# Optimization experiments

Measured on AMD Instinct MI355X. Metric: run time of the kernel, lower is better.

The kernel has to match this reference:

```python
import jax, jax.numpy as jnp
import numpy as np

N_NODES = 100000
N_EDGES = 1600000
D_IN = 64
D_OUT = 64


def setup_inputs() -> dict:
    key = jax.random.key(0)
    k1, k2, k3, k4 = jax.random.split(key, 4)
    x = jax.random.normal(k1, (N_NODES, D_IN), dtype=jnp.float32)
    edge_index = jax.random.randint(k2, (2, N_EDGES), 0, N_NODES, dtype=jnp.int64)
    W = jax.random.normal(k3, (D_OUT, D_IN), dtype=jnp.float32) * (1.0 / np.sqrt(D_IN))
    b = jax.random.normal(k4, (D_OUT,), dtype=jnp.float32) * 0.01
    return {"x": x, "edge_index": edge_index, "W": W, "b": b}


def reference(x, edge_index, W, b):
    num_nodes = x.shape[0]
    row, col = edge_index[0], edge_index[1]
    # degree of each node as a destination (scatter_add of ones over row)
    deg = jax.ops.segment_sum(jnp.ones(row.shape[0], dtype=x.dtype), row,
                              num_segments=num_nodes)
    # deg^-0.5 with inf (deg==0) replaced by 0
    deg_inv_sqrt = jnp.where(deg > 0, jax.lax.rsqrt(jnp.maximum(deg, 1.0)) * jnp.where(deg > 0, 1.0, 0.0), 0.0)
    deg_inv_sqrt = jnp.where(deg > 0, deg ** -0.5, 0.0)
    # gather source features, scale by source norm, scatter-add to destinations
    weighted = x[col] * deg_inv_sqrt[col][:, None]          # [E, D_IN]
    agg = jax.ops.segment_sum(weighted, row, num_segments=num_nodes)  # [N, D_IN]
    agg = agg * deg_inv_sqrt[:, None]
    # linear + relu (torch Linear: y = agg @ W.T + b)
    return jax.nn.relu(agg @ W.T + b)
```

## Files before the change

kernel.cpp:

```cpp
#include <hip/hip_runtime.h>

#define N_NODES 100000
#define N_EDGES 1600000
#define D 64

#define CSHIFT 7
#define CNODES 128
#define NCB 782
#define CAPC 2560
#define COLBITS 17
#define COLMASK 0x1FFFF

#define CHUNKA 2048
#define EPTA 8
#define NCHA 782
#define XBLKS 1563

#define CCUR_OFF   0
#define CPAIRS_OFF 3200
#define RS_OFF     8010880
#define DG_OFF     8410880
#define DINV_OFF   8810880
#define Y_OFF      9210880

typedef float fvec4 __attribute__((ext_vector_type(4)));
typedef __attribute__((ext_vector_type(8))) short bf16x8;
typedef __attribute__((ext_vector_type(4))) float f32x4;

__device__ __forceinline__ float bf2f(unsigned short u) {
    return __uint_as_float(((unsigned)u) << 16);
}
__device__ __forceinline__ unsigned f2bf(float f) {
    unsigned bits = __float_as_uint(f);
    return (bits + 0x7FFFu + ((bits >> 16) & 1u)) >> 16;
}

__global__ __launch_bounds__(256) void fat_kernel(
        const float* __restrict__ x, const float* __restrict__ W,
        const int* __restrict__ row, const int* __restrict__ col,
        int* __restrict__ ccur, int* __restrict__ cpairs,
        unsigned short* __restrict__ y) {
    __shared__ int lcnt[NCB];
    int t = threadIdx.x;
    if (blockIdx.x < XBLKS) {
        int wave = t >> 6, lane = t & 63;
        int n0w = blockIdx.x * 64 + wave * 16;
        if (n0w >= N_NODES) return;
        int lm = lane & 15;
        int g  = lane >> 4;
        bf16x8 ahi[2], alo[2];
        const float* xr = x + (size_t)(n0w + lm) * D + g * 8;
#pragma unroll
        for (int ks = 0; ks < 2; ++ks) {
            float4 fa = *(const float4*)(xr + ks * 32);
            float4 fb = *(const float4*)(xr + ks * 32 + 4);
            float f[8] = {fa.x, fa.y, fa.z, fa.w, fb.x, fb.y, fb.z, fb.w};
#pragma unroll
            for (int j = 0; j < 8; ++j) {
                unsigned hb = f2bf(f[j]);
                float r = f[j] - bf2f((unsigned short)hb);
                ahi[ks][j] = (short)hb;
                alo[ks][j] = (short)f2bf(r);
            }
        }
#pragma unroll
        for (int jt = 0; jt < 4; ++jt) {
            const float* wr = W + (size_t)(jt * 16 + lm) * D + g * 8;
            bf16x8 whi[2], wlo[2];
#pragma unroll
            for (int ks = 0; ks < 2; ++ks) {
                float4 fa = *(const float4*)(wr + ks * 32);
                float4 fb = *(const float4*)(wr + ks * 32 + 4);
                float f[8] = {fa.x, fa.y, fa.z, fa.w, fb.x, fb.y, fb.z, fb.w};
#pragma unroll
                for (int j = 0; j < 8; ++j) {
                    unsigned hb = f2bf(f[j]);
                    float r = f[j] - bf2f((unsigned short)hb);
                    whi[ks][j] = (short)hb;
                    wlo[ks][j] = (short)f2bf(r);
                }
            }
            f32x4 acc = {0.0f, 0.0f, 0.0f, 0.0f};
#pragma unroll
            for (int ks = 0; ks < 2; ++ks) {
                acc = __builtin_amdgcn_mfma_f32_16x16x32_bf16(ahi[ks], whi[ks], acc, 0, 0, 0);
                acc = __builtin_amdgcn_mfma_f32_16x16x32_bf16(alo[ks], whi[ks], acc, 0, 0, 0);
                acc = __builtin_amdgcn_mfma_f32_16x16x32_bf16(ahi[ks], wlo[ks], acc, 0, 0, 0);
            }
#pragma unroll
            for (int r = 0; r < 4; ++r) {
                int n = n0w + g * 4 + r;
                y[(size_t)n * D + jt * 16 + lm] = (unsigned short)f2bf(acc[r]);
            }
        }
    } else {
        int base = (blockIdx.x - XBLKS) * CHUNKA;
        for (int i = t; i < NCB; i += 256) lcnt[i] = 0;
        __syncthreads();
        int r[EPTA], c[EPTA], pos[EPTA];
#pragma unroll
        for (int i = 0; i < EPTA; ++i) {
            int e = base + i * 256 + t;
            if (e < N_EDGES) {
                r[i] = row[e];
                c[i] = col[e];
                pos[i] = atomicAdd(&lcnt[r[i] >> CSHIFT], 1);
            } else r[i] = -1;
        }
        __syncthreads();
        for (int i = t; i < NCB; i += 256) {
            int cc = lcnt[i];
            lcnt[i] = cc ? atomicAdd(&ccur[i], cc) : 0;
        }
        __syncthreads();
#pragma unroll
        for (int i = 0; i < EPTA; ++i) {
            if (r[i] >= 0) {
                int cb = r[i] >> CSHIFT;
                int p = lcnt[cb] + pos[i];
                if (p < CAPC)
                    cpairs[cb * CAPC + p] = ((r[i] & (CNODES - 1)) << COLBITS) | c[i];
            }
        }
    }
}

__global__ __launch_bounds__(512) void scatB_kernel(const int* __restrict__ ccur,
                                                    int* __restrict__ cpairs,
                                                    int* __restrict__ rs,
                                                    int* __restrict__ dg,
                                                    float* __restrict__ dinv) {
    __shared__ int epk[CAPC];
    __shared__ int hist[CNODES];
    __shared__ int sc[CNODES];
    __shared__ int cur[CNODES];
    int t = threadIdx.x;
    int cb = blockIdx.x;
    int cnt = ccur[cb]; if (cnt > CAPC) cnt = CAPC;
    int base = cb * CAPC;
    if (t < CNODES) hist[t] = 0;
    __syncthreads();
    for (int i = t; i < cnt; i += 512) {
        int p = cpairs[base + i];
        epk[i] = p;
        atomicAdd(&hist[p >> COLBITS], 1);
    }
    __syncthreads();
    if (t < CNODES) sc[t] = hist[t];
    __syncthreads();
    for (int off = 1; off < CNODES; off <<= 1) {
        int v = (t < CNODES && t >= off) ? sc[t - off] : 0;
        __syncthreads();
        if (t < CNODES) sc[t] += v;
        __syncthreads();
    }
    if (t < CNODES) {
        int ex = sc[t] - hist[t];
        cur[t] = ex;
        int n = (cb << CSHIFT) + t;
        if (n < N_NODES) {
            rs[n] = base + ex;
            dg[n] = hist[t];
            dinv[n] = (hist[t] > 0) ? rsqrtf((float)hist[t]) : 0.0f;
        }
    }
    __syncthreads();
    for (int i = t; i < cnt; i += 512) {
        int p = epk[i];
        int pos = atomicAdd(&cur[p >> COLBITS], 1);
        cpairs[base + pos] = p & COLMASK;
    }
}

__global__ __launch_bounds__(256) void mega_kernel(
        const int* __restrict__ cols, const int* __restrict__ rs,
        const int* __restrict__ dg, const float* __restrict__ dinv,
        const unsigned short* __restrict__ y,
        const float* __restrict__ bias, float* __restrict__ out) {
    int t = threadIdx.x;
    int wave = t >> 6, lane = t & 63;
    int g = lane >> 3, q = lane & 7;
    int n = blockIdx.x * 32 + wave * 8 + g;
    int s = rs[n], d = dg[n];
    float bj[8];
    {
        float4 b0 = *(const float4*)(bias + q * 8);
        float4 b1 = *(const float4*)(bias + q * 8 + 4);
        bj[0] = b0.x; bj[1] = b0.y; bj[2] = b0.z; bj[3] = b0.w;
        bj[4] = b1.x; bj[5] = b1.y; bj[6] = b1.z; bj[7] = b1.w;
    }
    float a[8];
#pragma unroll
    for (int j = 0; j < 8; ++j) a[j] = 0.0f;
    int c4[4];
#pragma unroll
    for (int u = 0; u < 4; ++u) c4[u] = (u < d) ? cols[s + u] : 0;
    for (int k = 0; k < d; k += 4) {
        uint4 v[4];
        float dvl[4];
#pragma unroll
        for (int u = 0; u < 4; ++u) {
            if (k + u < d) {
                int c = c4[u];
                dvl[u] = dinv[c];
                v[u] = *(const uint4*)(y + (size_t)c * D + q * 8);
            }
        }
#pragma unroll
        for (int u = 0; u < 4; ++u) {
            int e2 = k + 4 + u;
            c4[u] = (e2 < d) ? cols[s + e2] : 0;
        }
#pragma unroll
        for (int u = 0; u < 4; ++u) {
            if (k + u < d) {
                float dvu = dvl[u];
                a[0] = fmaf(dvu, __uint_as_float(v[u].x << 16),        a[0]);
                a[1] = fmaf(dvu, __uint_as_float(v[u].x & 0xffff0000u), a[1]);
                a[2] = fmaf(dvu, __uint_as_float(v[u].y << 16),        a[2]);
                a[3] = fmaf(dvu, __uint_as_float(v[u].y & 0xffff0000u), a[3]);
                a[4] = fmaf(dvu, __uint_as_float(v[u].z << 16),        a[4]);
                a[5] = fmaf(dvu, __uint_as_float(v[u].z & 0xffff0000u), a[5]);
                a[6] = fmaf(dvu, __uint_as_float(v[u].w << 16),        a[6]);
                a[7] = fmaf(dvu, __uint_as_float(v[u].w & 0xffff0000u), a[7]);
            }
        }
    }
    float dvn = dinv[n];
    fvec4 r0, r1;
    r0.x = fmaxf(fmaf(dvn, a[0], bj[0]), 0.0f);
    r0.y = fmaxf(fmaf(dvn, a[1], bj[1]), 0.0f);
    r0.z = fmaxf(fmaf(dvn, a[2], bj[2]), 0.0f);
    r0.w = fmaxf(fmaf(dvn, a[3], bj[3]), 0.0f);
    r1.x = fmaxf(fmaf(dvn, a[4], bj[4]), 0.0f);
    r1.y = fmaxf(fmaf(dvn, a[5], bj[5]), 0.0f);
    r1.z = fmaxf(fmaf(dvn, a[6], bj[6]), 0.0f);
    r1.w = fmaxf(fmaf(dvn, a[7], bj[7]), 0.0f);
    __builtin_nontemporal_store(r0, (fvec4*)(out + (size_t)n * D + q * 8));
    __builtin_nontemporal_store(r1, (fvec4*)(out + (size_t)n * D + q * 8 + 4));
}

extern "C" void kernel_launch(void* const* d_in, const int* in_sizes, int n_in,
                              void* d_out, int out_size, void* d_ws, size_t ws_size,
                              hipStream_t stream) {
    const float* x    = (const float*)d_in[0];
    const int*   eidx = (const int*)d_in[1];
    const float* W    = (const float*)d_in[2];
    const float* b    = (const float*)d_in[3];
    float* out = (float*)d_out;
    char* ws = (char*)d_ws;

    const int* row = eidx;
    const int* col = eidx + N_EDGES;

    int* ccur   = (int*)(ws + CCUR_OFF);
    int* cpairs = (int*)(ws + CPAIRS_OFF);
    int* rs     = (int*)(ws + RS_OFF);
    int* dg     = (int*)(ws + DG_OFF);
    float* dinv = (float*)(ws + DINV_OFF);
    unsigned short* y = (unsigned short*)(ws + Y_OFF);

    hipMemsetAsync(ccur, 0, NCB * sizeof(int), stream);
    fat_kernel<<<XBLKS + NCHA, 256, 0, stream>>>(x, W, row, col, ccur, cpairs, y);
    scatB_kernel<<<NCB, 512, 0, stream>>>(ccur, cpairs, rs, dg, dinv);
    mega_kernel<<<3125, 256, 0, stream>>>(cpairs, rs, dg, dinv, y, b, out);
}
```

Before: 169.9 us.

## Replace bucketed CSR build with global-atomic degree count, scan, and scatter

Replaces the two-level bucketed CSR construction (per-chunk LDS histograms into fixed-capacity coarse buckets, then a per-bucket local sort) with a global degree histogram made of global atomics, a three-kernel prefix scan, and a scatter pass that places each edge with a per-node global atomic. This removes the capacity limit and the intermediate packing, at the cost of three extra kernel launches and many contended global atomics on random node indices. The aggregation kernel's gather unroll also grows from 4 to 8 neighbours per step to keep more loads in flight, which raises register pressure.

Result: slower. 286.2 us (+68.5%).

```diff
diff --git a/kernel.cpp b/kernel.cpp
--- a/kernel.cpp
+++ b/kernel.cpp
@@ -2,26 +2,21 @@
 
 #define N_NODES 100000
 #define N_EDGES 1600000
+#define NE4 400000
 #define D 64
 
-#define CSHIFT 7
-#define CNODES 128
-#define NCB 782
-#define CAPC 2560
-#define COLBITS 17
-#define COLMASK 0x1FFFF
-
-#define CHUNKA 2048
-#define EPTA 8
-#define NCHA 782
 #define XBLKS 1563
-
-#define CCUR_OFF   0
-#define CPAIRS_OFF 3200
-#define RS_OFF     8010880
-#define DG_OFF     8410880
-#define DINV_OFF   8810880
-#define Y_OFF      9210880
+#define HBLKS 391
+#define NSB 391
+
+#define DG_OFF    0
+#define CUR_OFF   401408
+#define RS_OFF    802816
+#define DINV_OFF  1204224
+#define BSUM_OFF  1605632
+#define BOFF_OFF  1607232
+#define CP_OFF    1608832
+#define Y_OFF     8008832
 
 typedef float fvec4 __attribute__((ext_vector_type(4)));
 typedef __attribute__((ext_vector_type(8))) short bf16x8;
@@ -37,138 +32,150 @@
 
 __global__ __launch_bounds__(256) void fat_kernel(
         const float* __restrict__ x, const float* __restrict__ W,
-        const int* __restrict__ row, const int* __restrict__ col,
-        int* __restrict__ ccur, int* __restrict__ cpairs,
+        const int* __restrict__ row, int* __restrict__ dg,
         unsigned short* __restrict__ y) {
-    __shared__ int lcnt[NCB];
-    int t = threadIdx.x;
-    if (blockIdx.x < XBLKS) {
-        int wave = t >> 6, lane = t & 63;
-        int n0w = blockIdx.x * 64 + wave * 16;
-        if (n0w >= N_NODES) return;
-        int lm = lane & 15;
-        int g  = lane >> 4;
-        bf16x8 ahi[2], alo[2];
-        const float* xr = x + (size_t)(n0w + lm) * D + g * 8;
+    int t = threadIdx.x;
+    if (blockIdx.x < HBLKS) {
+        const int4* r4 = (const int4*)row;
+        int base4 = blockIdx.x * 1024;
+#pragma unroll
+        for (int i = 0; i < 4; ++i) {
+            int i4 = base4 + i * 256 + t;
+            if (i4 < NE4) {
+                int4 rv = r4[i4];
+                atomicAdd(&dg[rv.x], 1);
+                atomicAdd(&dg[rv.y], 1);
+                atomicAdd(&dg[rv.z], 1);
+                atomicAdd(&dg[rv.w], 1);
+            }
+        }
+        return;
+    }
+    int wave = t >> 6, lane = t & 63;
+    int n0w = (blockIdx.x - HBLKS) * 64 + wave * 16;
+    if (n0w >= N_NODES) return;
+    int lm = lane & 15;
+    int g  = lane >> 4;
+    bf16x8 ahi[2], alo[2];
+    const float* xr = x + (size_t)(n0w + lm) * D + g * 8;
+#pragma unroll
+    for (int ks = 0; ks < 2; ++ks) {
+        float4 fa = *(const float4*)(xr + ks * 32);
+        float4 fb = *(const float4*)(xr + ks * 32 + 4);
+        float f[8] = {fa.x, fa.y, fa.z, fa.w, fb.x, fb.y, fb.z, fb.w};
+#pragma unroll
+        for (int j = 0; j < 8; ++j) {
+            unsigned hb = f2bf(f[j]);
+            float r = f[j] - bf2f((unsigned short)hb);
+            ahi[ks][j] = (short)hb;
+            alo[ks][j] = (short)f2bf(r);
+        }
+    }
+#pragma unroll
+    for (int jt = 0; jt < 4; ++jt) {
+        const float* wr = W + (size_t)(jt * 16 + lm) * D + g * 8;
+        bf16x8 whi[2], wlo[2];
 #pragma unroll
         for (int ks = 0; ks < 2; ++ks) {
-            float4 fa = *(const float4*)(xr + ks * 32);
-            float4 fb = *(const float4*)(xr + ks * 32 + 4);
+            float4 fa = *(const float4*)(wr + ks * 32);
+            float4 fb = *(const float4*)(wr + ks * 32 + 4);
             float f[8] = {fa.x, fa.y, fa.z, fa.w, fb.x, fb.y, fb.z, fb.w};
 #pragma unroll
             for (int j = 0; j < 8; ++j) {
                 unsigned hb = f2bf(f[j]);
                 float r = f[j] - bf2f((unsigned short)hb);
-                ahi[ks][j] = (short)hb;
-                alo[ks][j] = (short)f2bf(r);
-            }
-        }
-#pragma unroll
-        for (int jt = 0; jt < 4; ++jt) {
-            const float* wr = W + (size_t)(jt * 16 + lm) * D + g * 8;
-            bf16x8 whi[2], wlo[2];
-#pragma unroll
-            for (int ks = 0; ks < 2; ++ks) {
-                float4 fa = *(const float4*)(wr + ks * 32);
-                float4 fb = *(const float4*)(wr + ks * 32 + 4);
-                float f[8] = {fa.x, fa.y, fa.z, fa.w, fb.x, fb.y, fb.z, fb.w};
-#pragma unroll
-                for (int j = 0; j < 8; ++j) {
-                    unsigned hb = f2bf(f[j]);
-                    float r = f[j] - bf2f((unsigned short)hb);
-                    whi[ks][j] = (short)hb;
-                    wlo[ks][j] = (short)f2bf(r);
-                }
-            }
-            f32x4 acc = {0.0f, 0.0f, 0.0f, 0.0f};
-#pragma unroll
-            for (int ks = 0; ks < 2; ++ks) {
-                acc = __builtin_amdgcn_mfma_f32_16x16x32_bf16(ahi[ks], whi[ks], acc, 0, 0, 0);
-                acc = __builtin_amdgcn_mfma_f32_16x16x32_bf16(alo[ks], whi[ks], acc, 0, 0, 0);
-                acc = __builtin_amdgcn_mfma_f32_16x16x32_bf16(ahi[ks], wlo[ks], acc, 0, 0, 0);
-            }
-#pragma unroll
-            for (int r = 0; r < 4; ++r) {
-                int n = n0w + g * 4 + r;
-                y[(size_t)n * D + jt * 16 + lm] = (unsigned short)f2bf(acc[r]);
-            }
-        }
-    } else {
-        int base = (blockIdx.x - XBLKS) * CHUNKA;
-        for (int i = t; i < NCB; i += 256) lcnt[i] = 0;
-        __syncthreads();
-        int r[EPTA], c[EPTA], pos[EPTA];
-#pragma unroll
-        for (int i = 0; i < EPTA; ++i) {
-            int e = base + i * 256 + t;
-            if (e < N_EDGES) {
-                r[i] = row[e];
-                c[i] = col[e];
-                pos[i] = atomicAdd(&lcnt[r[i] >> CSHIFT], 1);
-            } else r[i] = -1;
-        }
-        __syncthreads();
-        for (int i = t; i < NCB; i += 256) {
-            int cc = lcnt[i];
-            lcnt[i] = cc ? atomicAdd(&ccur[i], cc) : 0;
-        }
-        __syncthreads();
-#pragma unroll
-        for (int i = 0; i < EPTA; ++i) {
-            if (r[i] >= 0) {
-                int cb = r[i] >> CSHIFT;
-                int p = lcnt[cb] + pos[i];
-                if (p < CAPC)
-                    cpairs[cb * CAPC + p] = ((r[i] & (CNODES - 1)) << COLBITS) | c[i];
-            }
-        }
-    }
-}
-
-__global__ __launch_bounds__(512) void scatB_kernel(const int* __restrict__ ccur,
-                                                    int* __restrict__ cpairs,
+                whi[ks][j] = (short)hb;
+                wlo[ks][j] = (short)f2bf(r);
+            }
+        }
+        f32x4 acc = {0.0f, 0.0f, 0.0f, 0.0f};
+#pragma unroll
+        for (int ks = 0; ks < 2; ++ks) {
+            acc = __builtin_amdgcn_mfma_f32_16x16x32_bf16(ahi[ks], whi[ks], acc, 0, 0, 0);
+            acc = __builtin_amdgcn_mfma_f32_16x16x32_bf16(alo[ks], whi[ks], acc, 0, 0, 0);
+            acc = __builtin_amdgcn_mfma_f32_16x16x32_bf16(ahi[ks], wlo[ks], acc, 0, 0, 0);
+        }
+#pragma unroll
+        for (int r = 0; r < 4; ++r) {
+            int n = n0w + g * 4 + r;
+            y[(size_t)n * D + jt * 16 + lm] = (unsigned short)f2bf(acc[r]);
+        }
+    }
+}
+
+__global__ __launch_bounds__(256) void scan1_kernel(const int* __restrict__ dg,
+                                                    int* __restrict__ bsum) {
+    __shared__ int red[4];
+    int t = threadIdx.x;
+    int n = blockIdx.x * 256 + t;
+    int v = (n < N_NODES) ? dg[n] : 0;
+#pragma unroll
+    for (int m = 1; m < 64; m <<= 1) v += __shfl_xor(v, m);
+    if ((t & 63) == 0) red[t >> 6] = v;
+    __syncthreads();
+    if (t == 0) bsum[blockIdx.x] = red[0] + red[1] + red[2] + red[3];
+}
+
+__global__ __launch_bounds__(512) void scan2_kernel(const int* __restrict__ bsum,
+                                                    int* __restrict__ boff) {
+    __shared__ int ar[512];
+    int t = threadIdx.x;
+    int v = (t < NSB) ? bsum[t] : 0;
+    ar[t] = v;
+    __syncthreads();
+    for (int off = 1; off < 512; off <<= 1) {
+        int u = (t >= off) ? ar[t - off] : 0;
+        __syncthreads();
+        ar[t] += u;
+        __syncthreads();
+    }
+    if (t < NSB) boff[t] = ar[t] - v;
+}
+
+__global__ __launch_bounds__(256) void scan3_kernel(const int* __restrict__ dg,
+                                                    const int* __restrict__ boff,
                                                     int* __restrict__ rs,
-                                                    int* __restrict__ dg,
+                                                    int* __restrict__ cur,
                                                     float* __restrict__ dinv) {
-    __shared__ int epk[CAPC];
-    __shared__ int hist[CNODES];
-    __shared__ int sc[CNODES];
-    __shared__ int cur[CNODES];
-    int t = threadIdx.x;
-    int cb = blockIdx.x;
-    int cnt = ccur[cb]; if (cnt > CAPC) cnt = CAPC;
-    int base = cb * CAPC;
-    if (t < CNODES) hist[t] = 0;
+    __shared__ int ar[256];
+    int t = threadIdx.x;
+    int n = blockIdx.x * 256 + t;
+    int d = (n < N_NODES) ? dg[n] : 0;
+    ar[t] = d;
     __syncthreads();
-    for (int i = t; i < cnt; i += 512) {
-        int p = cpairs[base + i];
-        epk[i] = p;
-        atomicAdd(&hist[p >> COLBITS], 1);
-    }
-    __syncthreads();
-    if (t < CNODES) sc[t] = hist[t];
-    __syncthreads();
-    for (int off = 1; off < CNODES; off <<= 1) {
-        int v = (t < CNODES && t >= off) ? sc[t - off] : 0;
-        __syncthreads();
-        if (t < CNODES) sc[t] += v;
-        __syncthreads();
-    }
-    if (t < CNODES) {
-        int ex = sc[t] - hist[t];
-        cur[t] = ex;
-        int n = (cb << CSHIFT) + t;
-        if (n < N_NODES) {
-            rs[n] = base + ex;
-            dg[n] = hist[t];
-            dinv[n] = (hist[t] > 0) ? rsqrtf((float)hist[t]) : 0.0f;
-        }
-    }
-    __syncthreads();
-    for (int i = t; i < cnt; i += 512) {
-        int p = epk[i];
-        int pos = atomicAdd(&cur[p >> COLBITS], 1);
-        cpairs[base + pos] = p & COLMASK;
+    for (int off = 1; off < 256; off <<= 1) {
+        int u = (t >= off) ? ar[t - off] : 0;
+        __syncthreads();
+        ar[t] += u;
+        __syncthreads();
+    }
+    if (n < N_NODES) {
+        int r = boff[blockIdx.x] + ar[t] - d;
+        rs[n] = r;
+        cur[n] = r;
+        dinv[n] = (d > 0) ? rsqrtf((float)d) : 0.0f;
+    }
+}
+
+__global__ __launch_bounds__(256) void scat_kernel(const int* __restrict__ row,
+                                                   const int* __restrict__ col,
+                                                   int* __restrict__ cur,
+                                                   int* __restrict__ cpairs) {
+    int t = threadIdx.x;
+    const int4* r4 = (const int4*)row;
+    const int4* c4 = (const int4*)col;
+    int base4 = blockIdx.x * 1024;
+#pragma unroll
+    for (int i = 0; i < 4; ++i) {
+        int i4 = base4 + i * 256 + t;
+        if (i4 < NE4) {
+            int4 rv = r4[i4];
+            int4 cv = c4[i4];
+            int p0 = atomicAdd(&cur[rv.x], 1); cpairs[p0] = cv.x;
+            int p1 = atomicAdd(&cur[rv.y], 1); cpairs[p1] = cv.y;
+            int p2 = atomicAdd(&cur[rv.z], 1); cpairs[p2] = cv.z;
+            int p3 = atomicAdd(&cur[rv.w], 1); cpairs[p3] = cv.w;
+        }
     }
 }
 
@@ -192,36 +199,36 @@
     float a[8];
 #pragma unroll
     for (int j = 0; j < 8; ++j) a[j] = 0.0f;
-    int c4[4];
-#pragma unroll
-    for (int u = 0; u < 4; ++u) c4[u] = (u < d) ? cols[s + u] : 0;
-    for (int k = 0; k < d; k += 4) {
-        uint4 v[4];
-        float dvl[4];
-#pragma unroll
-        for (int u = 0; u < 4; ++u) {
+    int c8[8];
+#pragma unroll
+    for (int u = 0; u < 8; ++u) c8[u] = (u < d) ? cols[s + u] : 0;
+    for (int k = 0; k < d; k += 8) {
+        uint4 v[8];
+        float dv8[8];
+#pragma unroll
+        for (int u = 0; u < 8; ++u) {
             if (k + u < d) {
-                int c = c4[u];
-                dvl[u] = dinv[c];
+                int c = c8[u];
+                dv8[u] = dinv[c];
                 v[u] = *(const uint4*)(y + (size_t)c * D + q * 8);
             }
         }
 #pragma unroll
-        for (int u = 0; u < 4; ++u) {
-            int e2 = k + 4 + u;
-            c4[u] = (e2 < d) ? cols[s + e2] : 0;
-        }
-#pragma unroll
-        for (int u = 0; u < 4; ++u) {
+        for (int u = 0; u < 8; ++u) {
+            int e2 = k + 8 + u;
+            c8[u] = (e2 < d) ? cols[s + e2] : 0;
+        }
+#pragma unroll
+        for (int u = 0; u < 8; ++u) {
             if (k + u < d) {
-                float dvu = dvl[u];
-                a[0] = fmaf(dvu, __uint_as_float(v[u].x << 16),        a[0]);
+                float dvu = dv8[u];
+                a[0] = fmaf(dvu, __uint_as_float(v[u].x << 16),         a[0]);
                 a[1] = fmaf(dvu, __uint_as_float(v[u].x & 0xffff0000u), a[1]);
-                a[2] = fmaf(dvu, __uint_as_float(v[u].y << 16),        a[2]);
+                a[2] = fmaf(dvu, __uint_as_float(v[u].y << 16),         a[2]);
                 a[3] = fmaf(dvu, __uint_as_float(v[u].y & 0xffff0000u), a[3]);
-                a[4] = fmaf(dvu, __uint_as_float(v[u].z << 16),        a[4]);
+                a[4] = fmaf(dvu, __uint_as_float(v[u].z << 16),         a[4]);
                 a[5] = fmaf(dvu, __uint_as_float(v[u].z & 0xffff0000u), a[5]);
-                a[6] = fmaf(dvu, __uint_as_float(v[u].w << 16),        a[6]);
+                a[6] = fmaf(dvu, __uint_as_float(v[u].w << 16),         a[6]);
                 a[7] = fmaf(dvu, __uint_as_float(v[u].w & 0xffff0000u), a[7]);
             }
         }
@@ -253,15 +260,20 @@
     const int* row = eidx;
     const int* col = eidx + N_EDGES;
 
-    int* ccur   = (int*)(ws + CCUR_OFF);
-    int* cpairs = (int*)(ws + CPAIRS_OFF);
+    int* dg     = (int*)(ws + DG_OFF);
+    int* cur    = (int*)(ws + CUR_OFF);
     int* rs     = (int*)(ws + RS_OFF);
-    int* dg     = (int*)(ws + DG_OFF);
     float* dinv = (float*)(ws + DINV_OFF);
+    int* bsum   = (int*)(ws + BSUM_OFF);
+    int* boff   = (int*)(ws + BOFF_OFF);
+    int* cpairs = (int*)(ws + CP_OFF);
     unsigned short* y = (unsigned short*)(ws + Y_OFF);
 
-    hipMemsetAsync(ccur, 0, NCB * sizeof(int), stream);
-    fat_kernel<<<XBLKS + NCHA, 256, 0, stream>>>(x, W, row, col, ccur, cpairs, y);
-    scatB_kernel<<<NCB, 512, 0, stream>>>(ccur, cpairs, rs, dg, dinv);
+    hipMemsetAsync(dg, 0, N_NODES * sizeof(int), stream);
+    fat_kernel<<<HBLKS + XBLKS, 256, 0, stream>>>(x, W, row, dg, y);
+    scan1_kernel<<<NSB, 256, 0, stream>>>(dg, bsum);
+    scan2_kernel<<<1, 512, 0, stream>>>(bsum, boff);
+    scan3_kernel<<<NSB, 256, 0, stream>>>(dg, boff, rs, cur, dinv);
+    scat_kernel<<<HBLKS, 256, 0, stream>>>(row, col, cur, cpairs);
     mega_kernel<<<3125, 256, 0, stream>>>(cpairs, rs, dg, dinv, y, b, out);
 }
```

## Restructure edge bucketing into larger int4-vectorized blocks and unroll gather by eight

Applied to the files above, without the earlier changes.

The edge-bucketing part of the fused kernel now processes 8192 edges per block with int4 loads, and is placed before the matmul blocks so it is scheduled first. Each block counts per-bucket totals in a first pass, reserves global offsets once, then rereads the edges and scatters them, so per-block global atomics drop and more edges share each reservation. The gather loop in the aggregation kernel is unrolled from 4 to 8 neighbors to keep more loads in flight. The cost is reading row twice and fewer, longer scatter blocks, plus higher register pressure in the gather.

Measured after the change: 152.1 us. 10.5% less time.

```diff
diff --git a/kernel.cpp b/kernel.cpp
--- a/kernel.cpp
+++ b/kernel.cpp
@@ -2,6 +2,7 @@
 
 #define N_NODES 100000
 #define N_EDGES 1600000
+#define NE4 400000
 #define D 64
 
 #define CSHIFT 7
@@ -11,9 +12,8 @@
 #define COLBITS 17
 #define COLMASK 0x1FFFF
 
-#define CHUNKA 2048
-#define EPTA 8
-#define NCHA 782
+#define EPB 8192
+#define SBLKS 196
 #define XBLKS 1563
 
 #define CCUR_OFF   0
@@ -41,86 +41,100 @@
         int* __restrict__ ccur, int* __restrict__ cpairs,
         unsigned short* __restrict__ y) {
     __shared__ int lcnt[NCB];
+    __shared__ int lbase[NCB];
     int t = threadIdx.x;
-    if (blockIdx.x < XBLKS) {
-        int wave = t >> 6, lane = t & 63;
-        int n0w = blockIdx.x * 64 + wave * 16;
-        if (n0w >= N_NODES) return;
-        int lm = lane & 15;
-        int g  = lane >> 4;
-        bf16x8 ahi[2], alo[2];
-        const float* xr = x + (size_t)(n0w + lm) * D + g * 8;
+    if (blockIdx.x < SBLKS) {
+        const int4* r4 = (const int4*)row;
+        const int4* c4 = (const int4*)col;
+        int base4 = blockIdx.x * (EPB / 4);
+        for (int i = t; i < NCB; i += 256) lcnt[i] = 0;
+        __syncthreads();
+#pragma unroll
+        for (int i = 0; i < EPB / 1024; ++i) {
+            int i4 = base4 + i * 256 + t;
+            if (i4 < NE4) {
+                int4 rv = r4[i4];
+                atomicAdd(&lcnt[rv.x >> CSHIFT], 1);
+                atomicAdd(&lcnt[rv.y >> CSHIFT], 1);
+                atomicAdd(&lcnt[rv.z >> CSHIFT], 1);
+                atomicAdd(&lcnt[rv.w >> CSHIFT], 1);
+            }
+        }
+        __syncthreads();
+        for (int i = t; i < NCB; i += 256) {
+            int cc = lcnt[i];
+            lbase[i] = cc ? atomicAdd(&ccur[i], cc) : 0;
+            lcnt[i] = 0;
+        }
+        __syncthreads();
+#pragma unroll
+        for (int i = 0; i < EPB / 1024; ++i) {
+            int i4 = base4 + i * 256 + t;
+            if (i4 < NE4) {
+                int4 rv = r4[i4];
+                int4 cv = c4[i4];
+                int b0 = rv.x >> CSHIFT, b1 = rv.y >> CSHIFT;
+                int b2 = rv.z >> CSHIFT, b3 = rv.w >> CSHIFT;
+                int p0 = lbase[b0] + atomicAdd(&lcnt[b0], 1);
+                int p1 = lbase[b1] + atomicAdd(&lcnt[b1], 1);
+                int p2 = lbase[b2] + atomicAdd(&lcnt[b2], 1);
+                int p3 = lbase[b3] + atomicAdd(&lcnt[b3], 1);
+                if (p0 < CAPC) cpairs[(size_t)b0 * CAPC + p0] = ((rv.x & (CNODES - 1)) << COLBITS) | cv.x;
+                if (p1 < CAPC) cpairs[(size_t)b1 * CAPC + p1] = ((rv.y & (CNODES - 1)) << COLBITS) | cv.y;
+                if (p2 < CAPC) cpairs[(size_t)b2 * CAPC + p2] = ((rv.z & (CNODES - 1)) << COLBITS) | cv.z;
+                if (p3 < CAPC) cpairs[(size_t)b3 * CAPC + p3] = ((rv.w & (CNODES - 1)) << COLBITS) | cv.w;
+            }
+        }
+        return;
+    }
+    int wave = t >> 6, lane = t & 63;
+    int n0w = (blockIdx.x - SBLKS) * 64 + wave * 16;
+    if (n0w >= N_NODES) return;
+    int lm = lane & 15;
+    int g  = lane >> 4;
+    bf16x8 ahi[2], alo[2];
+    const float* xr = x + (size_t)(n0w + lm) * D + g * 8;
+#pragma unroll
+    for (int ks = 0; ks < 2; ++ks) {
+        float4 fa = *(const float4*)(xr + ks * 32);
+        float4 fb = *(const float4*)(xr + ks * 32 + 4);
+        float f[8] = {fa.x, fa.y, fa.z, fa.w, fb.x, fb.y, fb.z, fb.w};
+#pragma unroll
+        for (int j = 0; j < 8; ++j) {
+            unsigned hb = f2bf(f[j]);
+            float r = f[j] - bf2f((unsigned short)hb);
+            ahi[ks][j] = (short)hb;
+            alo[ks][j] = (short)f2bf(r);
+        }
+    }
+#pragma unroll
+    for (int jt = 0; jt < 4; ++jt) {
+        const float* wr = W + (size_t)(jt * 16 + lm) * D + g * 8;
+        bf16x8 whi[2], wlo[2];
 #pragma unroll
         for (int ks = 0; ks < 2; ++ks) {
-            float4 fa = *(const float4*)(xr + ks * 32);
-            float4 fb = *(const float4*)(xr + ks * 32 + 4);
+            float4 fa = *(const float4*)(wr + ks * 32);
+            float4 fb = *(const float4*)(wr + ks * 32 + 4);
             float f[8] = {fa.x, fa.y, fa.z, fa.w, fb.x, fb.y, fb.z, fb.w};
 #pragma unroll
             for (int j = 0; j < 8; ++j) {
                 unsigned hb = f2bf(f[j]);
                 float r = f[j] - bf2f((unsigned short)hb);
-                ahi[ks][j] = (short)hb;
-                alo[ks][j] = (short)f2bf(r);
-            }
-        }
-#pragma unroll
-        for (int jt = 0; jt < 4; ++jt) {
-            const float* wr = W + (size_t)(jt * 16 + lm) * D + g * 8;
-            bf16x8 whi[2], wlo[2];
-#pragma unroll
-            for (int ks = 0; ks < 2; ++ks) {
-                float4 fa = *(const float4*)(wr + ks * 32);
-                float4 fb = *(const float4*)(wr + ks * 32 + 4);
-                float f[8] = {fa.x, fa.y, fa.z, fa.w, fb.x, fb.y, fb.z, fb.w};
-#pragma unroll
-                for (int j = 0; j < 8; ++j) {
-                    unsigned hb = f2bf(f[j]);
-                    float r = f[j] - bf2f((unsigned short)hb);
-                    whi[ks][j] = (short)hb;
-                    wlo[ks][j] = (short)f2bf(r);
-                }
-            }
-            f32x4 acc = {0.0f, 0.0f, 0.0f, 0.0f};
-#pragma unroll
-            for (int ks = 0; ks < 2; ++ks) {
-                acc = __builtin_amdgcn_mfma_f32_16x16x32_bf16(ahi[ks], whi[ks], acc, 0, 0, 0);
-                acc = __builtin_amdgcn_mfma_f32_16x16x32_bf16(alo[ks], whi[ks], acc, 0, 0, 0);
-                acc = __builtin_amdgcn_mfma_f32_16x16x32_bf16(ahi[ks], wlo[ks], acc, 0, 0, 0);
-            }
-#pragma unroll
-            for (int r = 0; r < 4; ++r) {
-                int n = n0w + g * 4 + r;
-                y[(size_t)n * D + jt * 16 + lm] = (unsigned short)f2bf(acc[r]);
-            }
-        }
-    } else {
-        int base = (blockIdx.x - XBLKS) * CHUNKA;
-        for (int i = t; i < NCB; i += 256) lcnt[i] = 0;
-        __syncthreads();
-        int r[EPTA], c[EPTA], pos[EPTA];
-#pragma unroll
-        for (int i = 0; i < EPTA; ++i) {
-            int e = base + i * 256 + t;
-            if (e < N_EDGES) {
-                r[i] = row[e];
-                c[i] = col[e];
-                pos[i] = atomicAdd(&lcnt[r[i] >> CSHIFT], 1);
-            } else r[i] = -1;
-        }
-        __syncthreads();
-        for (int i = t; i < NCB; i += 256) {
-            int cc = lcnt[i];
-            lcnt[i] = cc ? atomicAdd(&ccur[i], cc) : 0;
-        }
-        __syncthreads();
-#pragma unroll
-        for (int i = 0; i < EPTA; ++i) {
-            if (r[i] >= 0) {
-                int cb = r[i] >> CSHIFT;
-                int p = lcnt[cb] + pos[i];
-                if (p < CAPC)
-                    cpairs[cb * CAPC + p] = ((r[i] & (CNODES - 1)) << COLBITS) | c[i];
-            }
+                whi[ks][j] = (short)hb;
+                wlo[ks][j] = (short)f2bf(r);
+            }
+        }
+        f32x4 acc = {0.0f, 0.0f, 0.0f, 0.0f};
+#pragma unroll
+        for (int ks = 0; ks < 2; ++ks) {
+            acc = __builtin_amdgcn_mfma_f32_16x16x32_bf16(ahi[ks], whi[ks], acc, 0, 0, 0);
+            acc = __builtin_amdgcn_mfma_f32_16x16x32_bf16(alo[ks], whi[ks], acc, 0, 0, 0);
+            acc = __builtin_amdgcn_mfma_f32_16x16x32_bf16(ahi[ks], wlo[ks], acc, 0, 0, 0);
+        }
+#pragma unroll
+        for (int r = 0; r < 4; ++r) {
+            int n = n0w + g * 4 + r;
+            y[(size_t)n * D + jt * 16 + lm] = (unsigned short)f2bf(acc[r]);
         }
     }
 }
@@ -192,36 +206,36 @@
     float a[8];
 #pragma unroll
     for (int j = 0; j < 8; ++j) a[j] = 0.0f;
-    int c4[4];
-#pragma unroll
-    for (int u = 0; u < 4; ++u) c4[u] = (u < d) ? cols[s + u] : 0;
-    for (int k = 0; k < d; k += 4) {
-        uint4 v[4];
-        float dvl[4];
-#pragma unroll
-        for (int u = 0; u < 4; ++u) {
+    int c8[8];
+#pragma unroll
+    for (int u = 0; u < 8; ++u) c8[u] = (u < d) ? cols[s + u] : 0;
+    for (int k = 0; k < d; k += 8) {
+        uint4 v[8];
+        float dv8[8];
+#pragma unroll
+        for (int u = 0; u < 8; ++u) {
             if (k + u < d) {
-                int c = c4[u];
-                dvl[u] = dinv[c];
+                int c = c8[u];
+                dv8[u] = dinv[c];
                 v[u] = *(const uint4*)(y + (size_t)c * D + q * 8);
             }
         }
 #pragma unroll
-        for (int u = 0; u < 4; ++u) {
-            int e2 = k + 4 + u;
-            c4[u] = (e2 < d) ? cols[s + e2] : 0;
-        }
-#pragma unroll
-        for (int u = 0; u < 4; ++u) {
+        for (int u = 0; u < 8; ++u) {
+            int e2 = k + 8 + u;
+            c8[u] = (e2 < d) ? cols[s + e2] : 0;
+        }
+#pragma unroll
+        for (int u = 0; u < 8; ++u) {
             if (k + u < d) {
-                float dvu = dvl[u];
-                a[0] = fmaf(dvu, __uint_as_float(v[u].x << 16),        a[0]);
+                float dvu = dv8[u];
+                a[0] = fmaf(dvu, __uint_as_float(v[u].x << 16),         a[0]);
                 a[1] = fmaf(dvu, __uint_as_float(v[u].x & 0xffff0000u), a[1]);
-                a[2] = fmaf(dvu, __uint_as_float(v[u].y << 16),        a[2]);
+                a[2] = fmaf(dvu, __uint_as_float(v[u].y << 16),         a[2]);
                 a[3] = fmaf(dvu, __uint_as_float(v[u].y & 0xffff0000u), a[3]);
-                a[4] = fmaf(dvu, __uint_as_float(v[u].z << 16),        a[4]);
+                a[4] = fmaf(dvu, __uint_as_float(v[u].z << 16),         a[4]);
                 a[5] = fmaf(dvu, __uint_as_float(v[u].z & 0xffff0000u), a[5]);
-                a[6] = fmaf(dvu, __uint_as_float(v[u].w << 16),        a[6]);
+                a[6] = fmaf(dvu, __uint_as_float(v[u].w << 16),         a[6]);
                 a[7] = fmaf(dvu, __uint_as_float(v[u].w & 0xffff0000u), a[7]);
             }
         }
@@ -261,7 +275,7 @@
     unsigned short* y = (unsigned short*)(ws + Y_OFF);
 
     hipMemsetAsync(ccur, 0, NCB * sizeof(int), stream);
-    fat_kernel<<<XBLKS + NCHA, 256, 0, stream>>>(x, W, row, col, ccur, cpairs, y);
+    fat_kernel<<<SBLKS + XBLKS, 256, 0, stream>>>(x, W, row, col, ccur, cpairs, y);
     scatB_kernel<<<NCB, 512, 0, stream>>>(ccur, cpairs, rs, dg, dinv);
     mega_kernel<<<3125, 256, 0, stream>>>(cpairs, rs, dg, dinv, y, b, out);
 }
```
